# Optimization experiments

Measured on AMD Instinct MI355X. Metric: run time of the kernel, lower is better.

The kernel has to match this reference:

```python
import jax, jax.numpy as jnp
import numpy as np

FEATS = 64
POS = 3
EDGE_ATTR = 4
M_DIM = 16
N_LAYERS = 3
EDGE_IN = 2 * FEATS + EDGE_ATTR + 1  # 133


def setup_inputs() -> dict:
    key = jax.random.key(0)
    ks = jax.random.split(key, 20)
    N, E = 50000, 800000
    x = jax.random.normal(ks[0], (N, FEATS + POS), dtype=jnp.float32)
    edge_index = jax.random.randint(ks[1], (2, E), 0, N, dtype=jnp.int64)
    edge_attr = jax.random.normal(ks[2], (E, EDGE_ATTR), dtype=jnp.float32)
    s = 0.02
    L = N_LAYERS
    inp = {
        "x": x, "edge_index": edge_index, "edge_attr": edge_attr,
        # edge_mlp: Linear(EDGE_IN, 2*EDGE_IN) -> SiLU -> Linear(2*EDGE_IN, M_DIM) -> SiLU
        "edge_w1": jax.random.normal(ks[3], (L, EDGE_IN, 2 * EDGE_IN), dtype=jnp.float32) * s,
        "edge_b1": jnp.zeros((L, 2 * EDGE_IN), dtype=jnp.float32),
        "edge_w2": jax.random.normal(ks[4], (L, 2 * EDGE_IN, M_DIM), dtype=jnp.float32) * s,
        "edge_b2": jnp.zeros((L, M_DIM), dtype=jnp.float32),
        # coors_mlp: Linear(M, 4M) -> SiLU -> Linear(4M, 1)
        "coors_w1": jax.random.normal(ks[5], (L, M_DIM, 4 * M_DIM), dtype=jnp.float32) * s,
        "coors_b1": jnp.zeros((L, 4 * M_DIM), dtype=jnp.float32),
        "coors_w2": jax.random.normal(ks[6], (L, 4 * M_DIM, 1), dtype=jnp.float32) * s,
        "coors_b2": jnp.zeros((L, 1), dtype=jnp.float32),
        # node_mlp: Linear(FEATS+M, 2*FEATS) -> SiLU -> Linear(2*FEATS, FEATS)
        "node_w1": jax.random.normal(ks[7], (L, FEATS + M_DIM, 2 * FEATS), dtype=jnp.float32) * s,
        "node_b1": jnp.zeros((L, 2 * FEATS), dtype=jnp.float32),
        "node_w2": jax.random.normal(ks[8], (L, 2 * FEATS, FEATS), dtype=jnp.float32) * s,
        "node_b2": jnp.zeros((L, FEATS), dtype=jnp.float32),
    }
    return inp


def _egnn_layer(x, edge_index, edge_attr,
                ew1, eb1, ew2, eb2, cw1, cb1, cw2, cb2, nw1, nb1, nw2, nb2):
    N = x.shape[0]
    feats, coors = x[:, :FEATS], x[:, FEATS:]
    src, dst = edge_index[0], edge_index[1]
    rel_coors = coors[src] - coors[dst]                       # [E, 3]
    rel_dist = jnp.sum(rel_coors ** 2, axis=-1, keepdims=True)  # [E, 1]
    ea = jnp.concatenate([edge_attr, rel_dist], axis=-1)      # [E, EDGE_ATTR+1]
    # PyG default flow source_to_target: x_i = x[dst], x_j = x[src]
    edge_in = jnp.concatenate([feats[dst], feats[src], ea], axis=-1)  # [E, EDGE_IN]
    h = jax.nn.silu(edge_in @ ew1 + eb1)
    m_ij = jax.nn.silu(h @ ew2 + eb2)                         # [E, M_DIM]
    coor_w = jax.nn.silu(m_ij @ cw1 + cb1) @ cw2 + cb2        # [E, 1]
    # aggregate (default 'add') over destination nodes
    m_i = jax.ops.segment_sum(m_ij, dst, num_segments=N)      # [N, M_DIM]
    coor_wi = jax.ops.segment_sum(coor_w, dst, num_segments=N)  # [N, 1]
    coor_ri = jax.ops.segment_sum(rel_coors, dst, num_segments=N)  # [N, 3]
    coors_out = coors + coor_wi * coor_ri
    node_in = jnp.concatenate([feats, m_i], axis=-1)
    hidden = jax.nn.silu(node_in @ nw1 + nb1) @ nw2 + nb2
    hidden_out = hidden + feats
    return jnp.concatenate([hidden_out, coors_out], axis=-1)


def reference(x, edge_index, edge_attr,
              edge_w1, edge_b1, edge_w2, edge_b2,
              coors_w1, coors_b1, coors_w2, coors_b2,
              node_w1, node_b1, node_w2, node_b2):
    for l in range(N_LAYERS):
        x = _egnn_layer(x, edge_index, edge_attr,
                        edge_w1[l], edge_b1[l], edge_w2[l], edge_b2[l],
                        coors_w1[l], coors_b1[l], coors_w2[l], coors_b2[l],
                        node_w1[l], node_b1[l], node_w2[l], node_b2[l])
    return x
```

## Files before the change

kernel.cpp:

```cpp
#include <hip/hip_runtime.h>
#include <hip/hip_bf16.h>

#define XDIM 67
#define EIN_D 133
#define H1 266
#define KP 160
#define KP_E 168
#define JP 320
#define JP_H 328
#define EPB 48

typedef __attribute__((ext_vector_type(8))) short bf16x8;
typedef __attribute__((ext_vector_type(4))) float f32x4;

__device__ __forceinline__ float silu_f(float x) { return x / (1.f + __expf(-x)); }

__device__ __forceinline__ unsigned short bf16_rne(float f) {
    unsigned int u = __float_as_uint(f);
    u += 0x7fffu + ((u >> 16) & 1u);
    return (unsigned short)(u >> 16);
}
__device__ __forceinline__ float bf16_to_f(unsigned short h) {
    return __uint_as_float(((unsigned int)h) << 16);
}
__device__ __forceinline__ void split2(float v, unsigned short& h, unsigned short& l) {
    h = bf16_rne(v);
    l = bf16_rne(v - bf16_to_f(h));
}

__global__ void zero_kernel(float* __restrict__ p, int n) {
    int n4 = n >> 2;
    float4* p4 = (float4*)p;
    for (int i = blockIdx.x * blockDim.x + threadIdx.x; i < n4; i += gridDim.x * blockDim.x)
        p4[i] = make_float4(0.f, 0.f, 0.f, 0.f);
    if (blockIdx.x == 0 && threadIdx.x == 0)
        for (int i = n4 * 4; i < n; ++i) p[i] = 0.f;
}

__global__ void copy_kernel(const float* __restrict__ src, float* __restrict__ dst, int n) {
    int n4 = n >> 2;
    const float4* s4 = (const float4*)src;
    float4* d4 = (float4*)dst;
    for (int i = blockIdx.x * blockDim.x + threadIdx.x; i < n4; i += gridDim.x * blockDim.x)
        d4[i] = s4[i];
    if (blockIdx.x == 0 && threadIdx.x == 0)
        for (int i = n4 * 4; i < n; ++i) dst[i] = src[i];
}

__global__ void prep_w1t(const float* __restrict__ ew1, unsigned short* __restrict__ whi,
                         unsigned short* __restrict__ wlo) {
    int idx = blockIdx.x * 256 + threadIdx.x;
    if (idx >= 3 * JP * KP) return;
    int l = idx / (JP * KP);
    int rem = idx - l * JP * KP;
    int j = rem / KP, k = rem - (rem / KP) * KP;
    float w = (j < H1 && k < EIN_D) ? ew1[((size_t)l * EIN_D + k) * H1 + j] : 0.f;
    unsigned short h = bf16_rne(w);
    whi[idx] = h;
    wlo[idx] = bf16_rne(w - bf16_to_f(h));
}

__global__ void prep_w2t(const float* __restrict__ ew2, unsigned short* __restrict__ w2tg) {
    int idx = blockIdx.x * 256 + threadIdx.x;
    if (idx >= 3 * 16 * JP_H) return;
    int l = idx / (16 * JP_H);
    int rem = idx - l * 16 * JP_H;
    int c = rem / JP_H, j = rem - (rem / JP_H) * JP_H;
    float w = (j < H1) ? ew2[((size_t)l * H1 + j) * 16 + c] : 0.f;
    unsigned short h = bf16_rne(w);
    w2tg[((size_t)l * 2 + 0) * 16 * JP_H + c * JP_H + j] = h;
    w2tg[((size_t)l * 2 + 1) * 16 * JP_H + c * JP_H + j] = bf16_rne(w - bf16_to_f(h));
}

__global__ void prep_b1(const float* __restrict__ b1, float* __restrict__ b1p) {
    int idx = blockIdx.x * 256 + threadIdx.x;
    if (idx >= 3 * JP) return;
    int l = idx / JP, j = idx - (idx / JP) * JP;
    b1p[idx] = (j < H1) ? b1[l * H1 + j] : 0.f;
}

__global__ __launch_bounds__(256, 4) void edge_kernel(
    const float* __restrict__ x,
    const int* __restrict__ eidx,
    const float* __restrict__ eattr,
    const unsigned short* __restrict__ w1hi,
    const unsigned short* __restrict__ w1lo,
    const float* __restrict__ b1p,
    const unsigned short* __restrict__ w2tg,
    const float* __restrict__ b2,
    const float* __restrict__ cw1, const float* __restrict__ cb1,
    const float* __restrict__ cw2, const float* __restrict__ cb2,
    float* __restrict__ m_i, float* __restrict__ cri, float* __restrict__ cwi,
    int E, int N)
{
    __shared__ __align__(16) unsigned short uA[2 * EPB * KP_E];
    __shared__ float mij[EPB][17];
    __shared__ float relc[EPB][4];
    __shared__ int dstl[EPB];
    __shared__ int srcl[EPB];

    unsigned short* ein_hi = uA;
    unsigned short* ein_lo = uA + EPB * KP_E;
    unsigned short* h_hi   = uA;

    const int tid = threadIdx.x;
    const int lane = tid & 63;
    const int w = tid >> 6;
    const int ge0 = blockIdx.x * EPB;

    if (tid < EPB) {
        int e = tid, ge = ge0 + e;
        if (ge < E) {
            int s = eidx[ge];
            int d = eidx[E + ge];
            dstl[e] = d; srcl[e] = s;
            const float* xs = x + (size_t)s * XDIM;
            const float* xd = x + (size_t)d * XDIM;
            float r0 = xs[64] - xd[64], r1 = xs[65] - xd[65], r2 = xs[66] - xd[66];
            relc[e][0] = r0; relc[e][1] = r1; relc[e][2] = r2;
            float dist = r0 * r0 + r1 * r1 + r2 * r2;
            unsigned short hh, hl;
            split2(dist, hh, hl);
            ein_hi[e * KP_E + 132] = hh;
            ein_lo[e * KP_E + 132] = hl;
        } else {
            dstl[e] = 0; srcl[e] = 0;
            relc[e][0] = relc[e][1] = relc[e][2] = 0.f;
            ein_hi[e * KP_E + 132] = 0;
            ein_lo[e * KP_E + 132] = 0;
        }
    }
    if (tid >= 64) {
        int t = tid - 64;
        int e = t >> 2, c = t & 3, ge = ge0 + e;
        float a = (ge < E) ? eattr[(size_t)ge * 4 + c] : 0.f;
        unsigned short hh, hl;
        split2(a, hh, hl);
        ein_hi[e * KP_E + 128 + c] = hh;
        ein_lo[e * KP_E + 128 + c] = hl;
    }
    for (int t = tid; t < EPB * 27; t += 256) {
        int e = t / 27, c = 133 + (t - (t / 27) * 27);
        ein_hi[e * KP_E + c] = 0;
        ein_lo[e * KP_E + c] = 0;
    }
    __syncthreads();

    {
        const int rquad = lane >> 4;
        const int c0 = (lane & 15) * 4;
        const int ebase = w * 12;
#pragma unroll
        for (int q = 0; q < 3; ++q) {
            int er = ebase + q * 4 + rquad;
            int nd = dstl[er];
            int ns = srcl[er];
            const float* xdr = x + (size_t)nd * XDIM;
            const float* xsr = x + (size_t)ns * XDIM;
            ushort4 dh, dl, sh, sl;
            split2(xdr[c0 + 0], dh.x, dl.x);
            split2(xdr[c0 + 1], dh.y, dl.y);
            split2(xdr[c0 + 2], dh.z, dl.z);
            split2(xdr[c0 + 3], dh.w, dl.w);
            split2(xsr[c0 + 0], sh.x, sl.x);
            split2(xsr[c0 + 1], sh.y, sl.y);
            split2(xsr[c0 + 2], sh.z, sl.z);
            split2(xsr[c0 + 3], sh.w, sl.w);
            *(ushort4*)&ein_hi[er * KP_E + c0]      = dh;
            *(ushort4*)&ein_lo[er * KP_E + c0]      = dl;
            *(ushort4*)&ein_hi[er * KP_E + 64 + c0] = sh;
            *(ushort4*)&ein_lo[er * KP_E + 64 + c0] = sl;
        }
    }
    __syncthreads();

    const int r16 = lane & 15, g4 = lane >> 4;
    const int jt0 = w * 5;

    f32x4 acc[5][3];
#pragma unroll
    for (int a = 0; a < 5; ++a)
#pragma unroll
        for (int b = 0; b < 3; ++b) acc[a][b] = (f32x4){0.f, 0.f, 0.f, 0.f};

#pragma unroll
    for (int kk = 0; kk < 5; ++kk) {
        const int ko = kk * 32 + g4 * 8;
        bf16x8 ah[3], al[3];
#pragma unroll
        for (int et = 0; et < 3; ++et) {
            ah[et] = *(const bf16x8*)&ein_hi[(et * 16 + r16) * KP_E + ko];
            al[et] = *(const bf16x8*)&ein_lo[(et * 16 + r16) * KP_E + ko];
        }
#pragma unroll
        for (int j5 = 0; j5 < 5; ++j5) {
            const size_t wo = (size_t)((jt0 + j5) * 16 + r16) * KP + ko;
            bf16x8 bh = *(const bf16x8*)&w1hi[wo];
            bf16x8 bl = *(const bf16x8*)&w1lo[wo];
#pragma unroll
            for (int et = 0; et < 3; ++et) {
                acc[j5][et] = __builtin_amdgcn_mfma_f32_16x16x32_bf16(ah[et], bh, acc[j5][et], 0, 0, 0);
                acc[j5][et] = __builtin_amdgcn_mfma_f32_16x16x32_bf16(al[et], bh, acc[j5][et], 0, 0, 0);
                acc[j5][et] = __builtin_amdgcn_mfma_f32_16x16x32_bf16(ah[et], bl, acc[j5][et], 0, 0, 0);
            }
        }
    }

    float b1v[5];
#pragma unroll
    for (int j5 = 0; j5 < 5; ++j5) b1v[j5] = b1p[(jt0 + j5) * 16 + r16];

    __syncthreads();

#pragma unroll
    for (int j5 = 0; j5 < 5; ++j5)
#pragma unroll
        for (int et = 0; et < 3; ++et)
#pragma unroll
            for (int r = 0; r < 4; ++r) {
                float hv = silu_f(acc[j5][et][r] + b1v[j5]);
                h_hi[(et * 16 + g4 * 4 + r) * JP_H + (jt0 + j5) * 16 + r16] = bf16_rne(hv);
            }
    __syncthreads();

    if (w < 3) {
        f32x4 acc2 = (f32x4){0.f, 0.f, 0.f, 0.f};
        const unsigned short* hrow = &h_hi[(w * 16 + r16) * JP_H];
        const unsigned short* w2h = &w2tg[(size_t)r16 * JP_H];
        const unsigned short* w2l = &w2tg[(size_t)(16 + r16) * JP_H];
#pragma unroll
        for (int kk = 0; kk < 10; ++kk) {
            const int ko = kk * 32 + g4 * 8;
            bf16x8 hf = *(const bf16x8*)&hrow[ko];
            bf16x8 wh = *(const bf16x8*)&w2h[ko];
            bf16x8 wl = *(const bf16x8*)&w2l[ko];
            acc2 = __builtin_amdgcn_mfma_f32_16x16x32_bf16(hf, wh, acc2, 0, 0, 0);
            acc2 = __builtin_amdgcn_mfma_f32_16x16x32_bf16(hf, wl, acc2, 0, 0, 0);
        }
        float b2v = b2[r16];
#pragma unroll
        for (int r = 0; r < 4; ++r) {
            int e = w * 16 + g4 * 4 + r;
            float m = silu_f(acc2[r] + b2v);
            mij[e][r16] = m;
            if (ge0 + e < E) atomicAdd(&m_i[(size_t)dstl[e] * 16 + r16], m);
        }
    }
    __syncthreads();

    {
        const int tj = tid & 15, te = tid >> 4;
        const int e0c = te * 3;
        float cacc[3][4];
#pragma unroll
        for (int i = 0; i < 3; ++i)
#pragma unroll
            for (int u = 0; u < 4; ++u) cacc[i][u] = 0.f;
#pragma unroll
        for (int k = 0; k < 16; ++k) {
            float4 wvv = *(const float4*)&cw1[k * 64 + tj * 4];
#pragma unroll
            for (int i = 0; i < 3; ++i) {
                float av = mij[e0c + i][k];
                cacc[i][0] += av * wvv.x;
                cacc[i][1] += av * wvv.y;
                cacc[i][2] += av * wvv.z;
                cacc[i][3] += av * wvv.w;
            }
        }
        float4 cb1v = *(const float4*)&cb1[tj * 4];
        float4 cw2v = *(const float4*)&cw2[tj * 4];
        float cb2v = cb2[0];
#pragma unroll
        for (int i = 0; i < 3; ++i) {
            float pw = silu_f(cacc[i][0] + cb1v.x) * cw2v.x
                     + silu_f(cacc[i][1] + cb1v.y) * cw2v.y
                     + silu_f(cacc[i][2] + cb1v.z) * cw2v.z
                     + silu_f(cacc[i][3] + cb1v.w) * cw2v.w;
            pw += __shfl_xor(pw, 1, 16);
            pw += __shfl_xor(pw, 2, 16);
            pw += __shfl_xor(pw, 4, 16);
            pw += __shfl_xor(pw, 8, 16);
            if (tj == 0) relc[e0c + i][3] = pw + cb2v;
        }
    }
    __syncthreads();

    if (tid < EPB * 4) {
        int e = tid >> 2, c = tid & 3;
        if (ge0 + e < E) {
            int d = dstl[e];
            if (c < 3) atomicAdd(&cri[(size_t)d * 3 + c], relc[e][c]);
            else       atomicAdd(&cwi[d], relc[e][3]);
        }
    }
}

__global__ __launch_bounds__(256) void node_kernel(
    const float* xin,
    const float* __restrict__ m_i,
    const float* __restrict__ cri,
    const float* __restrict__ cwi,
    const float* __restrict__ nw1, const float* __restrict__ nb1,
    const float* __restrict__ nw2, const float* __restrict__ nb2,
    float* xout, int N)
{
    __shared__ __align__(16) float nin[2][80];
    __shared__ __align__(16) float hid[2][128];
    const int half = threadIdx.x >> 7, r = threadIdx.x & 127;
    const int n = blockIdx.x * 2 + half;
    const bool on = (n < N);

    if (on) {
        if (r < 64)      nin[half][r] = xin[(size_t)n * XDIM + r];
        else if (r < 80) nin[half][r] = m_i[(size_t)n * 16 + (r - 64)];
    }
    __syncthreads();
    if (on) {
        float h = nb1[r];
#pragma unroll
        for (int k = 0; k < 80; k += 4) {
            float4 a = *(const float4*)&nin[half][k];
            h += a.x * nw1[k * 128 + r] + a.y * nw1[(k + 1) * 128 + r]
               + a.z * nw1[(k + 2) * 128 + r] + a.w * nw1[(k + 3) * 128 + r];
        }
        hid[half][r] = silu_f(h);
    }
    __syncthreads();
    if (on) {
        if (r < 64) {
            float o = nb2[r];
#pragma unroll
            for (int k = 0; k < 128; k += 4) {
                float4 a = *(const float4*)&hid[half][k];
                o += a.x * nw2[k * 64 + r] + a.y * nw2[(k + 1) * 64 + r]
                   + a.z * nw2[(k + 2) * 64 + r] + a.w * nw2[(k + 3) * 64 + r];
            }
            xout[(size_t)n * XDIM + r] = o + nin[half][r];
        } else if (r < 67) {
            int c = r - 64;
            xout[(size_t)n * XDIM + r] =
                xin[(size_t)n * XDIM + r] + cwi[n] * cri[(size_t)n * 3 + c];
        }
    }
}

extern "C" void kernel_launch(void* const* d_in, const int* in_sizes, int n_in,
                              void* d_out, int out_size, void* d_ws, size_t ws_size,
                              hipStream_t stream) {
    const float* x     = (const float*)d_in[0];
    const int*   eidx  = (const int*)d_in[1];
    const float* eattr = (const float*)d_in[2];
    const float* ew1   = (const float*)d_in[3];
    const float* eb1   = (const float*)d_in[4];
    const float* ew2   = (const float*)d_in[5];
    const float* eb2   = (const float*)d_in[6];
    const float* cw1   = (const float*)d_in[7];
    const float* cb1   = (const float*)d_in[8];
    const float* cw2   = (const float*)d_in[9];
    const float* cb2   = (const float*)d_in[10];
    const float* nw1   = (const float*)d_in[11];
    const float* nb1   = (const float*)d_in[12];
    const float* nw2   = (const float*)d_in[13];
    const float* nb2   = (const float*)d_in[14];

    const int N = in_sizes[0] / XDIM;
    const int E = in_sizes[1] / 2;

    float* acc  = (float*)d_ws;
    float* m_i  = acc;
    float* cri  = acc + (size_t)N * 16;
    float* cwi  = acc + (size_t)N * 19;
    unsigned short* w1hi = (unsigned short*)(acc + (size_t)N * 20);
    unsigned short* w1lo = w1hi + (size_t)3 * JP * KP;
    unsigned short* w2tg = w1lo + (size_t)3 * JP * KP;
    float* b1p = (float*)(w2tg + (size_t)3 * 2 * 16 * JP_H);

    float* xwork = (float*)d_out;

    copy_kernel<<<2048, 256, 0, stream>>>(x, xwork, N * XDIM);
    prep_w1t<<<(3 * JP * KP + 255) / 256, 256, 0, stream>>>(ew1, w1hi, w1lo);
    prep_w2t<<<(3 * 16 * JP_H + 255) / 256, 256, 0, stream>>>(ew2, w2tg);
    prep_b1<<<(3 * JP + 255) / 256, 256, 0, stream>>>(eb1, b1p);

    for (int l = 0; l < 3; ++l) {
        zero_kernel<<<1024, 256, 0, stream>>>(acc, N * 20);
        edge_kernel<<<(E + EPB - 1) / EPB, 256, 0, stream>>>(
            xwork, eidx, eattr,
            w1hi + (size_t)l * JP * KP, w1lo + (size_t)l * JP * KP,
            b1p + (size_t)l * JP,
            w2tg + (size_t)l * 2 * 16 * JP_H,
            eb2 + (size_t)l * 16,
            cw1 + (size_t)l * 16 * 64, cb1 + (size_t)l * 64,
            cw2 + (size_t)l * 64, cb2 + l,
            m_i, cri, cwi, E, N);
        node_kernel<<<(N + 1) / 2, 256, 0, stream>>>(
            xwork, m_i, cri, cwi,
            nw1 + (size_t)l * 80 * 128, nb1 + (size_t)l * 128,
            nw2 + (size_t)l * 128 * 64, nb2 + (size_t)l * 64,
            xwork, N);
    }
}
```

Before: 1.890 ms.

## Use MFMA for coords MLP, packed bf16 conversion, fuse zeroing into node kernel

Several changes land together. The coordinate MLP's first layer now runs as a bf16 MFMA on a pre-transposed cw1, instead of scalar FMAs on fp32 m_ij staged in shared memory. The hi/lo bf16 split uses a packed hardware conversion with vectorized LDS stores, and the first-layer MFMA operands are swapped so each lane's accumulators land contiguously, allowing packed uint2 stores of the hidden activations. The per-layer zero kernel is removed: the accumulators are zeroed once alongside the initial copy and then cleared by the node kernel after use. The coordinate MLP input is rounded to single bf16, which slightly reduces precision.

```diff
diff --git a/kernel.cpp b/kernel.cpp
--- a/kernel.cpp
+++ b/kernel.cpp
@@ -8,10 +8,13 @@
 #define KP_E 168
 #define JP 320
 #define JP_H 328
+#define MSTR 40
 #define EPB 48
 
 typedef __attribute__((ext_vector_type(8))) short bf16x8;
 typedef __attribute__((ext_vector_type(4))) float f32x4;
+typedef __attribute__((ext_vector_type(2))) float f32x2;
+typedef __attribute__((ext_vector_type(2))) __bf16 b16x2;
 
 __device__ __forceinline__ float silu_f(float x) { return x / (1.f + __expf(-x)); }
 
@@ -23,28 +26,25 @@
 __device__ __forceinline__ float bf16_to_f(unsigned short h) {
     return __uint_as_float(((unsigned int)h) << 16);
 }
-__device__ __forceinline__ void split2(float v, unsigned short& h, unsigned short& l) {
-    h = bf16_rne(v);
-    l = bf16_rne(v - bf16_to_f(h));
-}
-
-__global__ void zero_kernel(float* __restrict__ p, int n) {
-    int n4 = n >> 2;
-    float4* p4 = (float4*)p;
-    for (int i = blockIdx.x * blockDim.x + threadIdx.x; i < n4; i += gridDim.x * blockDim.x)
-        p4[i] = make_float4(0.f, 0.f, 0.f, 0.f);
-    if (blockIdx.x == 0 && threadIdx.x == 0)
-        for (int i = n4 * 4; i < n; ++i) p[i] = 0.f;
-}
-
-__global__ void copy_kernel(const float* __restrict__ src, float* __restrict__ dst, int n) {
-    int n4 = n >> 2;
+__device__ __forceinline__ unsigned int packbf2(float a, float b) {
+    b16x2 c = __builtin_convertvector((f32x2){a, b}, b16x2);
+    unsigned int u; __builtin_memcpy(&u, &c, 4); return u;
+}
+
+__global__ void copy_zero_kernel(const float* __restrict__ src, float* __restrict__ dst,
+                                 int n, float* __restrict__ z, int nz) {
+    int n4 = n >> 2, nz4 = nz >> 2;
     const float4* s4 = (const float4*)src;
     float4* d4 = (float4*)dst;
+    float4* z4 = (float4*)z;
     for (int i = blockIdx.x * blockDim.x + threadIdx.x; i < n4; i += gridDim.x * blockDim.x)
         d4[i] = s4[i];
-    if (blockIdx.x == 0 && threadIdx.x == 0)
+    for (int i = blockIdx.x * blockDim.x + threadIdx.x; i < nz4; i += gridDim.x * blockDim.x)
+        z4[i] = make_float4(0.f, 0.f, 0.f, 0.f);
+    if (blockIdx.x == 0 && threadIdx.x == 0) {
         for (int i = n4 * 4; i < n; ++i) dst[i] = src[i];
+        for (int i = nz4 * 4; i < nz; ++i) z[i] = 0.f;
+    }
 }
 
 __global__ void prep_w1t(const float* __restrict__ ew1, unsigned short* __restrict__ whi,
@@ -79,6 +79,15 @@
     b1p[idx] = (j < H1) ? b1[l * H1 + j] : 0.f;
 }
 
+__global__ void prep_cw1t(const float* __restrict__ cw1, unsigned short* __restrict__ cw1t) {
+    int idx = blockIdx.x * 256 + threadIdx.x;
+    if (idx >= 3 * 64 * 32) return;
+    int l = idx / (64 * 32);
+    int rem = idx - l * 64 * 32;
+    int j = rem >> 5, c = rem & 31;
+    cw1t[idx] = (c < 16) ? bf16_rne(cw1[(size_t)l * 16 * 64 + c * 64 + j]) : (unsigned short)0;
+}
+
 __global__ __launch_bounds__(256, 4) void edge_kernel(
     const float* __restrict__ x,
     const int* __restrict__ eidx,
@@ -88,16 +97,16 @@
     const float* __restrict__ b1p,
     const unsigned short* __restrict__ w2tg,
     const float* __restrict__ b2,
-    const float* __restrict__ cw1, const float* __restrict__ cb1,
+    const unsigned short* __restrict__ cw1t,
+    const float* __restrict__ cb1,
     const float* __restrict__ cw2, const float* __restrict__ cb2,
     float* __restrict__ m_i, float* __restrict__ cri, float* __restrict__ cwi,
     int E, int N)
 {
     __shared__ __align__(16) unsigned short uA[2 * EPB * KP_E];
-    __shared__ float mij[EPB][17];
+    __shared__ __align__(16) unsigned short mij_bf[EPB * MSTR];
     __shared__ float relc[EPB][4];
-    __shared__ int dstl[EPB];
-    __shared__ int srcl[EPB];
+    __shared__ int dstl[EPB], srcl[EPB];
 
     unsigned short* ein_hi = uA;
     unsigned short* ein_lo = uA + EPB * KP_E;
@@ -107,6 +116,7 @@
     const int lane = tid & 63;
     const int w = tid >> 6;
     const int ge0 = blockIdx.x * EPB;
+    const int r16 = lane & 15, g4 = lane >> 4;
 
     if (tid < EPB) {
         int e = tid, ge = ge0 + e;
@@ -119,10 +129,9 @@
             float r0 = xs[64] - xd[64], r1 = xs[65] - xd[65], r2 = xs[66] - xd[66];
             relc[e][0] = r0; relc[e][1] = r1; relc[e][2] = r2;
             float dist = r0 * r0 + r1 * r1 + r2 * r2;
-            unsigned short hh, hl;
-            split2(dist, hh, hl);
+            unsigned short hh = bf16_rne(dist);
             ein_hi[e * KP_E + 132] = hh;
-            ein_lo[e * KP_E + 132] = hl;
+            ein_lo[e * KP_E + 132] = bf16_rne(dist - bf16_to_f(hh));
         } else {
             dstl[e] = 0; srcl[e] = 0;
             relc[e][0] = relc[e][1] = relc[e][2] = 0.f;
@@ -134,47 +143,56 @@
         int t = tid - 64;
         int e = t >> 2, c = t & 3, ge = ge0 + e;
         float a = (ge < E) ? eattr[(size_t)ge * 4 + c] : 0.f;
-        unsigned short hh, hl;
-        split2(a, hh, hl);
+        unsigned short hh = bf16_rne(a);
         ein_hi[e * KP_E + 128 + c] = hh;
-        ein_lo[e * KP_E + 128 + c] = hl;
+        ein_lo[e * KP_E + 128 + c] = bf16_rne(a - bf16_to_f(hh));
     }
     for (int t = tid; t < EPB * 27; t += 256) {
         int e = t / 27, c = 133 + (t - (t / 27) * 27);
         ein_hi[e * KP_E + c] = 0;
         ein_lo[e * KP_E + c] = 0;
     }
+    if (tid < 192) {
+        int e = tid >> 2, q = tid & 3;
+        uint2 zz; zz.x = 0u; zz.y = 0u;
+        *(uint2*)&mij_bf[e * MSTR + 16 + q * 4] = zz;
+    }
     __syncthreads();
 
     {
-        const int rquad = lane >> 4;
-        const int c0 = (lane & 15) * 4;
+        const int rquad = g4;
+        const int c0 = r16 * 4;
         const int ebase = w * 12;
 #pragma unroll
         for (int q = 0; q < 3; ++q) {
             int er = ebase + q * 4 + rquad;
-            int nd = dstl[er];
-            int ns = srcl[er];
-            const float* xdr = x + (size_t)nd * XDIM;
-            const float* xsr = x + (size_t)ns * XDIM;
-            ushort4 dh, dl, sh, sl;
-            split2(xdr[c0 + 0], dh.x, dl.x);
-            split2(xdr[c0 + 1], dh.y, dl.y);
-            split2(xdr[c0 + 2], dh.z, dl.z);
-            split2(xdr[c0 + 3], dh.w, dl.w);
-            split2(xsr[c0 + 0], sh.x, sl.x);
-            split2(xsr[c0 + 1], sh.y, sl.y);
-            split2(xsr[c0 + 2], sh.z, sl.z);
-            split2(xsr[c0 + 3], sh.w, sl.w);
-            *(ushort4*)&ein_hi[er * KP_E + c0]      = dh;
-            *(ushort4*)&ein_lo[er * KP_E + c0]      = dl;
-            *(ushort4*)&ein_hi[er * KP_E + 64 + c0] = sh;
-            *(ushort4*)&ein_lo[er * KP_E + 64 + c0] = sl;
-        }
-    }
-    __syncthreads();
-
-    const int r16 = lane & 15, g4 = lane >> 4;
+            const float* xdr = x + (size_t)dstl[er] * XDIM;
+            const float* xsr = x + (size_t)srcl[er] * XDIM;
+            float d0 = xdr[c0], d1 = xdr[c0 + 1], d2 = xdr[c0 + 2], d3 = xdr[c0 + 3];
+            float s0 = xsr[c0], s1 = xsr[c0 + 1], s2 = xsr[c0 + 2], s3 = xsr[c0 + 3];
+            unsigned int dh01 = packbf2(d0, d1), dh23 = packbf2(d2, d3);
+            unsigned int sh01 = packbf2(s0, s1), sh23 = packbf2(s2, s3);
+            float dl0 = d0 - __uint_as_float(dh01 << 16);
+            float dl1 = d1 - __uint_as_float(dh01 & 0xffff0000u);
+            float dl2 = d2 - __uint_as_float(dh23 << 16);
+            float dl3 = d3 - __uint_as_float(dh23 & 0xffff0000u);
+            float sl0 = s0 - __uint_as_float(sh01 << 16);
+            float sl1 = s1 - __uint_as_float(sh01 & 0xffff0000u);
+            float sl2 = s2 - __uint_as_float(sh23 << 16);
+            float sl3 = s3 - __uint_as_float(sh23 & 0xffff0000u);
+            uint2 vh, vl;
+            vh.x = dh01; vh.y = dh23;
+            vl.x = packbf2(dl0, dl1); vl.y = packbf2(dl2, dl3);
+            *(uint2*)&ein_hi[er * KP_E + c0] = vh;
+            *(uint2*)&ein_lo[er * KP_E + c0] = vl;
+            vh.x = sh01; vh.y = sh23;
+            vl.x = packbf2(sl0, sl1); vl.y = packbf2(sl2, sl3);
+            *(uint2*)&ein_hi[er * KP_E + 64 + c0] = vh;
+            *(uint2*)&ein_lo[er * KP_E + 64 + c0] = vl;
+        }
+    }
+    __syncthreads();
+
     const int jt0 = w * 5;
 
     f32x4 acc[5][3];
@@ -199,28 +217,35 @@
             bf16x8 bl = *(const bf16x8*)&w1lo[wo];
 #pragma unroll
             for (int et = 0; et < 3; ++et) {
-                acc[j5][et] = __builtin_amdgcn_mfma_f32_16x16x32_bf16(ah[et], bh, acc[j5][et], 0, 0, 0);
-                acc[j5][et] = __builtin_amdgcn_mfma_f32_16x16x32_bf16(al[et], bh, acc[j5][et], 0, 0, 0);
-                acc[j5][et] = __builtin_amdgcn_mfma_f32_16x16x32_bf16(ah[et], bl, acc[j5][et], 0, 0, 0);
+                acc[j5][et] = __builtin_amdgcn_mfma_f32_16x16x32_bf16(bh, ah[et], acc[j5][et], 0, 0, 0);
+                acc[j5][et] = __builtin_amdgcn_mfma_f32_16x16x32_bf16(bl, ah[et], acc[j5][et], 0, 0, 0);
+                acc[j5][et] = __builtin_amdgcn_mfma_f32_16x16x32_bf16(bh, al[et], acc[j5][et], 0, 0, 0);
             }
         }
     }
 
-    float b1v[5];
-#pragma unroll
-    for (int j5 = 0; j5 < 5; ++j5) b1v[j5] = b1p[(jt0 + j5) * 16 + r16];
-
-    __syncthreads();
-
+    float4 b1v[5];
 #pragma unroll
     for (int j5 = 0; j5 < 5; ++j5)
-#pragma unroll
-        for (int et = 0; et < 3; ++et)
-#pragma unroll
-            for (int r = 0; r < 4; ++r) {
-                float hv = silu_f(acc[j5][et][r] + b1v[j5]);
-                h_hi[(et * 16 + g4 * 4 + r) * JP_H + (jt0 + j5) * 16 + r16] = bf16_rne(hv);
-            }
+        b1v[j5] = *(const float4*)&b1p[(jt0 + j5) * 16 + g4 * 4];
+
+    __syncthreads();
+
+#pragma unroll
+    for (int j5 = 0; j5 < 5; ++j5) {
+#pragma unroll
+        for (int et = 0; et < 3; ++et) {
+            f32x4 a = acc[j5][et];
+            float h0 = silu_f(a[0] + b1v[j5].x);
+            float h1 = silu_f(a[1] + b1v[j5].y);
+            float h2 = silu_f(a[2] + b1v[j5].z);
+            float h3 = silu_f(a[3] + b1v[j5].w);
+            uint2 uu;
+            uu.x = packbf2(h0, h1);
+            uu.y = packbf2(h2, h3);
+            *(uint2*)&h_hi[(et * 16 + r16) * JP_H + (jt0 + j5) * 16 + g4 * 4] = uu;
+        }
+    }
     __syncthreads();
 
     if (w < 3) {
@@ -242,46 +267,45 @@
         for (int r = 0; r < 4; ++r) {
             int e = w * 16 + g4 * 4 + r;
             float m = silu_f(acc2[r] + b2v);
-            mij[e][r16] = m;
+            mij_bf[e * MSTR + r16] = bf16_rne(m);
             if (ge0 + e < E) atomicAdd(&m_i[(size_t)dstl[e] * 16 + r16], m);
         }
     }
     __syncthreads();
 
-    {
-        const int tj = tid & 15, te = tid >> 4;
-        const int e0c = te * 3;
-        float cacc[3][4];
-#pragma unroll
-        for (int i = 0; i < 3; ++i)
-#pragma unroll
-            for (int u = 0; u < 4; ++u) cacc[i][u] = 0.f;
-#pragma unroll
-        for (int k = 0; k < 16; ++k) {
-            float4 wvv = *(const float4*)&cw1[k * 64 + tj * 4];
-#pragma unroll
-            for (int i = 0; i < 3; ++i) {
-                float av = mij[e0c + i][k];
-                cacc[i][0] += av * wvv.x;
-                cacc[i][1] += av * wvv.y;
-                cacc[i][2] += av * wvv.z;
-                cacc[i][3] += av * wvv.w;
-            }
-        }
-        float4 cb1v = *(const float4*)&cb1[tj * 4];
-        float4 cw2v = *(const float4*)&cw2[tj * 4];
-        float cb2v = cb2[0];
-#pragma unroll
-        for (int i = 0; i < 3; ++i) {
-            float pw = silu_f(cacc[i][0] + cb1v.x) * cw2v.x
-                     + silu_f(cacc[i][1] + cb1v.y) * cw2v.y
-                     + silu_f(cacc[i][2] + cb1v.z) * cw2v.z
-                     + silu_f(cacc[i][3] + cb1v.w) * cw2v.w;
-            pw += __shfl_xor(pw, 1, 16);
-            pw += __shfl_xor(pw, 2, 16);
-            pw += __shfl_xor(pw, 4, 16);
-            pw += __shfl_xor(pw, 8, 16);
-            if (tj == 0) relc[e0c + i][3] = pw + cb2v;
+    if (w < 3) {
+        bf16x8 afrag = *(const bf16x8*)&mij_bf[(w * 16 + r16) * MSTR + g4 * 8];
+        f32x4 cacc[4];
+#pragma unroll
+        for (int jt = 0; jt < 4; ++jt) {
+            bf16x8 bfrag = *(const bf16x8*)&cw1t[(jt * 16 + r16) * 32 + g4 * 8];
+            cacc[jt] = __builtin_amdgcn_mfma_f32_16x16x32_bf16(afrag, bfrag,
+                        (f32x4){0.f, 0.f, 0.f, 0.f}, 0, 0, 0);
+        }
+        float pw0 = 0.f, pw1 = 0.f, pw2 = 0.f, pw3 = 0.f;
+#pragma unroll
+        for (int jt = 0; jt < 4; ++jt) {
+            float cb = cb1[jt * 16 + r16];
+            float cw = cw2[jt * 16 + r16];
+            pw0 += silu_f(cacc[jt][0] + cb) * cw;
+            pw1 += silu_f(cacc[jt][1] + cb) * cw;
+            pw2 += silu_f(cacc[jt][2] + cb) * cw;
+            pw3 += silu_f(cacc[jt][3] + cb) * cw;
+        }
+#pragma unroll
+        for (int s = 1; s < 16; s <<= 1) {
+            pw0 += __shfl_xor(pw0, s, 16);
+            pw1 += __shfl_xor(pw1, s, 16);
+            pw2 += __shfl_xor(pw2, s, 16);
+            pw3 += __shfl_xor(pw3, s, 16);
+        }
+        if (r16 == 0) {
+            float cb2v = cb2[0];
+            int e = w * 16 + g4 * 4;
+            relc[e + 0][3] = pw0 + cb2v;
+            relc[e + 1][3] = pw1 + cb2v;
+            relc[e + 2][3] = pw2 + cb2v;
+            relc[e + 3][3] = pw3 + cb2v;
         }
     }
     __syncthreads();
@@ -298,9 +322,9 @@
 
 __global__ __launch_bounds__(256) void node_kernel(
     const float* xin,
-    const float* __restrict__ m_i,
-    const float* __restrict__ cri,
-    const float* __restrict__ cwi,
+    float* __restrict__ m_i,
+    float* __restrict__ cri,
+    float* __restrict__ cwi,
     const float* __restrict__ nw1, const float* __restrict__ nb1,
     const float* __restrict__ nw2, const float* __restrict__ nb2,
     float* xout, int N)
@@ -342,6 +366,12 @@
             xout[(size_t)n * XDIM + r] =
                 xin[(size_t)n * XDIM + r] + cwi[n] * cri[(size_t)n * 3 + c];
         }
+    }
+    __syncthreads();
+    if (on) {
+        if (r < 16)      m_i[(size_t)n * 16 + r] = 0.f;
+        else if (r < 19) cri[(size_t)n * 3 + (r - 16)] = 0.f;
+        else if (r == 19) cwi[n] = 0.f;
     }
 }
 
@@ -371,27 +401,29 @@
     float* m_i  = acc;
     float* cri  = acc + (size_t)N * 16;
     float* cwi  = acc + (size_t)N * 19;
-    unsigned short* w1hi = (unsigned short*)(acc + (size_t)N * 20);
+    float* b1p  = acc + (size_t)N * 20;
+    unsigned short* w1hi = (unsigned short*)(b1p + (size_t)3 * JP);
     unsigned short* w1lo = w1hi + (size_t)3 * JP * KP;
     unsigned short* w2tg = w1lo + (size_t)3 * JP * KP;
-    float* b1p = (float*)(w2tg + (size_t)3 * 2 * 16 * JP_H);
+    unsigned short* cw1t = w2tg + (size_t)3 * 2 * 16 * JP_H;
 
     float* xwork = (float*)d_out;
 
-    copy_kernel<<<2048, 256, 0, stream>>>(x, xwork, N * XDIM);
+    copy_zero_kernel<<<2048, 256, 0, stream>>>(x, xwork, N * XDIM, acc, N * 20);
     prep_w1t<<<(3 * JP * KP + 255) / 256, 256, 0, stream>>>(ew1, w1hi, w1lo);
     prep_w2t<<<(3 * 16 * JP_H + 255) / 256, 256, 0, stream>>>(ew2, w2tg);
     prep_b1<<<(3 * JP + 255) / 256, 256, 0, stream>>>(eb1, b1p);
+    prep_cw1t<<<(3 * 64 * 32 + 255) / 256, 256, 0, stream>>>(cw1, cw1t);
 
     for (int l = 0; l < 3; ++l) {
-        zero_kernel<<<1024, 256, 0, stream>>>(acc, N * 20);
         edge_kernel<<<(E + EPB - 1) / EPB, 256, 0, stream>>>(
             xwork, eidx, eattr,
             w1hi + (size_t)l * JP * KP, w1lo + (size_t)l * JP * KP,
             b1p + (size_t)l * JP,
             w2tg + (size_t)l * 2 * 16 * JP_H,
             eb2 + (size_t)l * 16,
-            cw1 + (size_t)l * 16 * 64, cb1 + (size_t)l * 64,
+            cw1t + (size_t)l * 64 * 32,
+            cb1 + (size_t)l * 64,
             cw2 + (size_t)l * 64, cb2 + l,
             m_i, cri, cwi, E, N);
         node_kernel<<<(N + 1) / 2, 256, 0, stream>>>(
```

Measured after the change: 1.807 ms. -4.4%, faster.
